# Performance work log

Hardware: AMD Instinct MI355X
Metric: run time of the kernel (lower is better)

The kernel has to match this reference:

```python
import jax, jax.numpy as jnp
import numpy as np

B, S, SK = 4, 1024, 1024
Q_IN, KV_IN = 1024, 1024
G, DQ, DV = 16, 64, 64
OUT = Q_IN
EPS = 1e-5


def setup_inputs() -> dict:
    key = jax.random.key(0)
    ks = jax.random.split(key, 12)
    s_q = 1.0 / np.sqrt(Q_IN)
    s_kv = 1.0 / np.sqrt(KV_IN)
    s_p = 1.0 / np.sqrt(G * DV)
    return {
        "Q": jax.random.normal(ks[0], (B, S, Q_IN), jnp.float32),
        "KV": jax.random.normal(ks[1], (B, SK, KV_IN), jnp.float32),
        "Wq": jax.random.normal(ks[2], (G * DQ, Q_IN), jnp.float32) * s_q,
        "bq": jax.random.normal(ks[3], (G * DQ,), jnp.float32) * s_q,
        "Wk": jax.random.normal(ks[4], (G * DQ, KV_IN), jnp.float32) * s_kv,
        "bk": jax.random.normal(ks[5], (G * DQ,), jnp.float32) * s_kv,
        "Wv": jax.random.normal(ks[6], (G * DV, KV_IN), jnp.float32) * s_kv,
        "bv": jax.random.normal(ks[7], (G * DV,), jnp.float32) * s_kv,
        "Wp": jax.random.normal(ks[8], (OUT, G * DV), jnp.float32) * s_p,
        "bp": jax.random.normal(ks[9], (OUT,), jnp.float32) * s_p,
        "gamma": jnp.ones((OUT,), jnp.float32),
        "beta": jnp.zeros((OUT,), jnp.float32),
    }


def reference(Q, KV, Wq, bq, Wk, bk, Wv, bv, Wp, bp, gamma, beta):
    b, s, _ = Q.shape
    sk = KV.shape[1]
    inv_sqrt_dim = DQ ** (-0.5)

    # projections
    q = Q @ Wq.T + bq            # [b, s, G*DQ]
    k = KV @ Wk.T + bk           # [b, sk, G*DQ]
    v = KV @ Wv.T + bv           # [b, sk, G*DV]

    # q/k: group is the SLOW axis; v: group is the FAST axis (faithful to source)
    q = q.reshape(b, s, G, DQ)               # [b, s, g, d]
    k = k.reshape(b, sk, G, DQ)              # [b, sk, g, d]
    v = v.reshape(b, sk, DV, G)              # [b, sk, d, g]

    logits = jnp.einsum('bsgd,btgd->bgst', q, k) * inv_sqrt_dim  # [b, g, s, sk]
    scores = jax.nn.softmax(logits, axis=-1)
    attn = jnp.einsum('bgst,btdg->bgsd', scores, v)              # [b, g, s, dv]

    # flatten as (dv, g): feature index = d*G + g  (faithful to source permute)
    attn = attn.transpose(0, 2, 3, 1).reshape(b, s, DV * G)
    out = attn @ Wp.T + bp + Q

    # LayerNorm
    mu = out.mean(axis=-1, keepdims=True)
    var = out.var(axis=-1, keepdims=True)
    out = (out - mu) * jax.lax.rsqrt(var + EPS) * gamma + beta

    return out, scores.reshape(b * G, s, sk)
```

## Files before the change

### kernel.cpp

```cpp
#include <hip/hip_runtime.h>

typedef __attribute__((ext_vector_type(8))) short short8;
typedef __attribute__((ext_vector_type(4))) short s16x4;
typedef __attribute__((ext_vector_type(4))) float f32x4;
typedef __attribute__((ext_vector_type(2))) unsigned u32x2;

static __device__ __forceinline__ short f2bf(float x) {
  union { float f; unsigned u; } v; v.f = x;
  unsigned r = (v.u + 0x7fffu + ((v.u >> 16) & 1u)) >> 16;
  return (short)r;
}
static __device__ __forceinline__ unsigned cvtpk(float lo, float hi) {
  unsigned r;
  asm("v_cvt_pk_bf16_f32 %0, %1, %2" : "=v"(r) : "v"(lo), "v"(hi));
  return r;
}

static __device__ __forceinline__ void gld16(const short* g, short* l) {
  __builtin_amdgcn_global_load_lds(
      (const __attribute__((address_space(1))) unsigned*)g,
      (__attribute__((address_space(3))) unsigned*)l, 16, 0, 0);
}

static __device__ __forceinline__ void conv8(const float* __restrict__ src,
                                             short* __restrict__ dst, int i,
                                             float scale) {
  const f32x4* s = (const f32x4*)(src + (long)i * 8);
  f32x4 a = s[0], b = s[1];
  short8 o;
  o[0] = f2bf(a[0] * scale); o[1] = f2bf(a[1] * scale);
  o[2] = f2bf(a[2] * scale); o[3] = f2bf(a[3] * scale);
  o[4] = f2bf(b[0] * scale); o[5] = f2bf(b[1] * scale);
  o[6] = f2bf(b[2] * scale); o[7] = f2bf(b[3] * scale);
  *(short8*)(dst + (long)i * 8) = o;
}

__global__ __launch_bounds__(256) void prep(
    const float* __restrict__ Q, const float* __restrict__ KV,
    const float* __restrict__ Wq, const float* __restrict__ Wk,
    const float* __restrict__ Wv, const float* __restrict__ Wp,
    const float* __restrict__ bq,
    short* __restrict__ Qb, short* __restrict__ KVb,
    short* __restrict__ Wqb, short* __restrict__ Wkb,
    short* __restrict__ Wvb, short* __restrict__ Wpb,
    float* __restrict__ bqs) {
  const int blk = blockIdx.x, tid = threadIdx.x;
  if (blk < 2048) {
    conv8(Q, Qb, blk * 256 + tid, 1.f);
  } else if (blk < 4096) {
    conv8(KV, KVb, (blk - 2048) * 256 + tid, 1.f);
  } else if (blk < 4608) {
    conv8(Wq, Wqb, (blk - 4096) * 256 + tid, 0.125f);
  } else if (blk < 5120) {
    conv8(Wk, Wkb, (blk - 4608) * 256 + tid, 1.f);
  } else if (blk < 5632) {
    conv8(Wv, Wvb, (blk - 5120) * 256 + tid, 1.f);
  } else if (blk < 6656) {
    __shared__ float row[1024];
    const long o = blk - 5632;
    *(f32x4*)&row[tid * 4] = *(const f32x4*)(Wp + o * 1024 + tid * 4);
    __syncthreads();
    const int f0 = tid * 4;
    s16x4 t;
#pragma unroll
    for (int j = 0; j < 4; ++j) {
      int f = f0 + j;
      t[j] = f2bf(row[((f & 63) << 4) + (f >> 6)]);
    }
    *(s16x4*)(Wpb + o * 1024 + f0) = t;
  } else {
    int i = (blk - 6656) * 256 + tid;
    bqs[i] = bq[i] * 0.125f;
  }
}

template <typename OutT>
static __device__ __forceinline__ void gemm_core(
    const short* __restrict__ A, const short* __restrict__ B,
    OutT* __restrict__ C, const float* __restrict__ bias,
    const float* __restrict__ resid, int bm, int bn, int omode,
    short* Sm) {
  const int tid = threadIdx.x, lane = tid & 63, wave = tid >> 6;
  const int fr = lane & 15, khi = lane >> 4;
  const int wr = wave >> 1, wc = wave & 1;

  f32x4 acc[4][4];
#pragma unroll
  for (int m = 0; m < 4; ++m)
#pragma unroll
    for (int n = 0; n < 4; ++n) acc[m][n] = (f32x4){0.f, 0.f, 0.f, 0.f};

  auto stage = [&](int buf, int k0) {
    short* Asb = Sm + buf * 16384;
    short* Bsb = Asb + 8192;
#pragma unroll
    for (int it = 0; it < 4; ++it) {
      int l = it * 256 + tid;
      int r = l >> 3, c = (l & 7) ^ (r & 7);
      gld16(A + (long)(bm + r) * 1024 + k0 + c * 8, &Asb[l * 8]);
      gld16(B + (long)(bn + r) * 1024 + k0 + c * 8, &Bsb[l * 8]);
    }
  };

  stage(0, 0);
  __syncthreads();
  int cur = 0;
  for (int k0 = 0; k0 < 1024; k0 += 64) {
    if (k0 < 960) stage(cur ^ 1, k0 + 64);
    const short* Asb = Sm + cur * 16384;
    const short* Bsb = Asb + 8192;
#pragma unroll
    for (int ks = 0; ks < 64; ks += 32) {
      const int cc = (ks >> 3) + khi;
      short8 af[4], bf[4];
#pragma unroll
      for (int m = 0; m < 4; ++m) {
        const int ar = wr * 64 + m * 16 + fr;
        af[m] = *(const short8*)&Asb[ar * 64 + ((cc ^ (ar & 7)) * 8)];
      }
#pragma unroll
      for (int n = 0; n < 4; ++n) {
        const int br = wc * 64 + n * 16 + fr;
        bf[n] = *(const short8*)&Bsb[br * 64 + ((cc ^ (br & 7)) * 8)];
      }
#pragma unroll
      for (int m = 0; m < 4; ++m)
#pragma unroll
        for (int n = 0; n < 4; ++n)
          acc[m][n] = __builtin_amdgcn_mfma_f32_16x16x32_bf16(af[m], bf[n],
                                                              acc[m][n], 0, 0, 0);
    }
    __syncthreads();
    cur ^= 1;
  }

  const int col0 = fr, row0 = khi * 4;
  if constexpr (sizeof(OutT) == 2) {
#pragma unroll
    for (int m = 0; m < 4; ++m) {
#pragma unroll
      for (int n = 0; n < 4; ++n) {
        const int dgl = wc * 64 + n * 16 + col0;
        const float bi = bias[bn + dgl];
#pragma unroll
        for (int i = 0; i < 4; ++i) {
          const int tl = wr * 64 + m * 16 + row0 + i;
          const int a = (omode == 1) ? (dgl * 136 + tl) : (tl * 136 + dgl);
          Sm[a] = f2bf(acc[m][n][i] + bi);
        }
      }
    }
    __syncthreads();
    short* Cs = (short*)C;
#pragma unroll
    for (int it = 0; it < 8; ++it) {
      const int ch = it * 256 + tid;
      const int r = ch >> 4, cchunk = ch & 15;
      short8 v8 = *(const short8*)&Sm[r * 136 + cchunk * 8];
      long addr;
      if (omode == 0)
        addr = (long)(bm + r) * 1024 + bn + cchunk * 8;
      else
        addr = ((long)(bm >> 10) << 20) + ((long)(bn + r) << 10) + (bm & 1023) +
               cchunk * 8;
      *(short8*)(Cs + addr) = v8;
    }
  } else {
#pragma unroll
    for (int m = 0; m < 4; ++m) {
#pragma unroll
      for (int n = 0; n < 4; ++n) {
        const int gcol = bn + wc * 64 + n * 16 + col0;
        const float bi = bias[gcol];
#pragma unroll
        for (int i = 0; i < 4; ++i) {
          const int grow = bm + wr * 64 + m * 16 + row0 + i;
          float v = acc[m][n][i] + bi;
          if (resid) v += resid[(long)grow * 1024 + gcol];
          C[(long)grow * 1024 + gcol] = v;
        }
      }
    }
  }
}

__global__ __launch_bounds__(256, 2) void proj_all(
    const short* __restrict__ Qb, const short* __restrict__ KVb,
    const short* __restrict__ Wqb, const short* __restrict__ Wkb,
    const short* __restrict__ Wvb,
    const float* __restrict__ bqs, const float* __restrict__ bk,
    const float* __restrict__ bv,
    short* __restrict__ qb, short* __restrict__ kb, short* __restrict__ vt) {
  __shared__ short Sm[32768];
  int bid = blockIdx.x;
  int swz = (bid & 7) * 96 + (bid >> 3);
  const int seg = swz >> 8, local = swz & 255;
  const int bm = (local >> 3) * 128, bn = (local & 7) * 128;
  if (seg == 0)
    gemm_core<short>(Qb, Wqb, qb, bqs, nullptr, bm, bn, 0, Sm);
  else if (seg == 1)
    gemm_core<short>(KVb, Wkb, kb, bk, nullptr, bm, bn, 0, Sm);
  else
    gemm_core<short>(KVb, Wvb, vt, bv, nullptr, bm, bn, 1, Sm);
}

__global__ __launch_bounds__(256, 2) void out_gemm(
    const short* __restrict__ at, const short* __restrict__ Wpb,
    const float* __restrict__ bp, const float* __restrict__ Q,
    float* __restrict__ pre) {
  __shared__ short Sm[32768];
  int bid = blockIdx.x;
  int swz = (bid & 7) * 32 + (bid >> 3);
  const int bm = (swz >> 3) * 128, bn = (swz & 7) * 128;
  gemm_core<float>(at, Wpb, pre, bp, Q, bm, bn, 0, Sm);
}

__global__ __launch_bounds__(512, 4) void fused_attn(
    const short* __restrict__ qb,
    const short* __restrict__ kb,
    const short* __restrict__ vt,
    float* __restrict__ scores,
    short* __restrict__ at) {
  constexpr int LP = 72;
  __shared__ short Ks[2][64 * 64];
  __shared__ short Vs[2][64 * 64];
  __shared__ short Ps[128 * LP];

  int bid = blockIdx.x;
  bid = (bid & 7) * 64 + (bid >> 3);
  const int z = bid >> 3, b = z >> 4, g = z & 15;
  const int q0 = (bid & 7) * 128;

  const int tid = threadIdx.x, lane = tid & 63, w = tid >> 6;
  const int fr = lane & 15, khi = lane >> 4;
  const long bqk = (long)b << 20;
  const int qr = q0 + w * 16;

  const short* qrow = qb + bqk + (long)(qr + fr) * 1024 + g * 64 + khi * 8;
  const short8 aq0 = *(const short8*)qrow;
  const short8 aq1 = *(const short8*)(qrow + 32);
  const short* kgp = kb + bqk + g * 64;
  const short* vgp = vt + bqk;

  auto stageK = [&](int buf, int t0) {
    int r = tid >> 3, c = (tid & 7) ^ ((tid >> 5) & 7);
    gld16(kgp + (long)(t0 + r) * 1024 + c * 8, &Ks[buf][tid * 8]);
  };
  auto stageV = [&](int buf, int t0) {
    int r = tid >> 3, c = (tid & 7) ^ (r & 7);
    gld16(vgp + ((long)(r * 16 + g) << 10) + t0 + c * 8, &Vs[buf][tid * 8]);
  };

  const int xk = fr & 7;

  float s4[4] = {0.f, 0.f, 0.f, 0.f};
  stageK(0, 0);
  __syncthreads();
  int cur = 0;
  for (int t0 = 0; t0 < 1024; t0 += 64) {
    if (t0 < 960) stageK(cur ^ 1, t0 + 64);
    f32x4 sacc[4];
#pragma unroll
    for (int nf = 0; nf < 4; ++nf) sacc[nf] = (f32x4){0.f, 0.f, 0.f, 0.f};
#pragma unroll
    for (int nf = 0; nf < 4; ++nf) {
      const int r2 = fr * 4 + nf;
      short8 b0 = *(const short8*)&Ks[cur][r2 * 64 + ((khi ^ xk) * 8)];
      short8 b1 = *(const short8*)&Ks[cur][r2 * 64 + (((khi + 4) ^ xk) * 8)];
      sacc[nf] = __builtin_amdgcn_mfma_f32_16x16x32_bf16(aq0, b0, sacc[nf], 0, 0, 0);
      sacc[nf] = __builtin_amdgcn_mfma_f32_16x16x32_bf16(aq1, b1, sacc[nf], 0, 0, 0);
    }
#pragma unroll
    for (int nf = 0; nf < 4; ++nf)
#pragma unroll
      for (int i = 0; i < 4; ++i) s4[i] += __expf(sacc[nf][i]);
    __syncthreads();
    cur ^= 1;
  }
  float inv4[4];
#pragma unroll
  for (int i = 0; i < 4; ++i) {
    float s = s4[i];
    s += __shfl_xor(s, 1);
    s += __shfl_xor(s, 2);
    s += __shfl_xor(s, 4);
    s += __shfl_xor(s, 8);
    inv4[i] = 1.f / s;
  }

  f32x4 pacc[4];
#pragma unroll
  for (int nv = 0; nv < 4; ++nv) pacc[nv] = (f32x4){0.f, 0.f, 0.f, 0.f};

  stageK(0, 0);
  stageV(0, 0);
  __syncthreads();
  cur = 0;
  for (int t0 = 0; t0 < 1024; t0 += 64) {
    if (t0 < 960) {
      stageK(cur ^ 1, t0 + 64);
      stageV(cur ^ 1, t0 + 64);
    }
    f32x4 sacc[4];
#pragma unroll
    for (int nf = 0; nf < 4; ++nf) sacc[nf] = (f32x4){0.f, 0.f, 0.f, 0.f};
#pragma unroll
    for (int nf = 0; nf < 4; ++nf) {
      const int r2 = fr * 4 + nf;
      short8 b0 = *(const short8*)&Ks[cur][r2 * 64 + ((khi ^ xk) * 8)];
      short8 b1 = *(const short8*)&Ks[cur][r2 * 64 + (((khi + 4) ^ xk) * 8)];
      sacc[nf] = __builtin_amdgcn_mfma_f32_16x16x32_bf16(aq0, b0, sacc[nf], 0, 0, 0);
      sacc[nf] = __builtin_amdgcn_mfma_f32_16x16x32_bf16(aq1, b1, sacc[nf], 0, 0, 0);
    }
#pragma unroll
    for (int i = 0; i < 4; ++i) {
      f32x4 o;
#pragma unroll
      for (int nf = 0; nf < 4; ++nf)
        o[nf] = __expf(sacc[nf][i]) * inv4[i];
      const int row = khi * 4 + i;
      __builtin_nontemporal_store(
          o, (f32x4*)&scores[((long)z << 20) + ((long)(qr + row) << 10) + t0 + fr * 4]);
      u32x2 pp;
      pp[0] = cvtpk(o[0], o[1]);
      pp[1] = cvtpk(o[2], o[3]);
      *(u32x2*)&Ps[(w * 16 + row) * LP + fr * 4] = pp;
    }

#pragma unroll
    for (int ks = 0; ks < 64; ks += 32) {
      const int cc = (ks >> 3) + khi;
      short8 ap = *(const short8*)&Ps[(w * 16 + fr) * LP + ks + khi * 8];
#pragma unroll
      for (int nv = 0; nv < 4; ++nv) {
        const int dr = nv * 16 + fr;
        short8 bvv = *(const short8*)&Vs[cur][dr * 64 + ((cc ^ (dr & 7)) * 8)];
        pacc[nv] = __builtin_amdgcn_mfma_f32_16x16x32_bf16(ap, bvv, pacc[nv], 0, 0, 0);
      }
    }
    __syncthreads();
    cur ^= 1;
  }

#pragma unroll
  for (int nv = 0; nv < 4; ++nv)
#pragma unroll
    for (int i = 0; i < 4; ++i)
      Ps[(w * 16 + khi * 4 + i) * LP + nv * 16 + fr] = f2bf(pacc[nv][i]);
  const long atbase = bqk + ((long)qr << 10) + g * 64;
#pragma unroll
  for (int it = 0; it < 2; ++it) {
    const int ch = it * 64 + lane;
    const int row = ch >> 3, fc = ch & 7;
    s16x4 lo = *(const s16x4*)&Ps[(w * 16 + row) * LP + fc * 8];
    s16x4 hi = *(const s16x4*)&Ps[(w * 16 + row) * LP + fc * 8 + 4];
    short8 v8;
    v8[0] = lo[0]; v8[1] = lo[1]; v8[2] = lo[2]; v8[3] = lo[3];
    v8[4] = hi[0]; v8[5] = hi[1]; v8[6] = hi[2]; v8[7] = hi[3];
    *(short8*)(at + atbase + ((long)row << 10) + fc * 8) = v8;
  }
}

__global__ __launch_bounds__(256) void layernorm_rows(const float* __restrict__ X,
                                                      const float* __restrict__ gamma,
                                                      const float* __restrict__ beta,
                                                      float* __restrict__ O) {
  const int row = blockIdx.x * 4 + (threadIdx.x >> 6);
  const int lane = threadIdx.x & 63;
  const float* x = X + (long)row * 1024 + lane * 4;
  f32x4 v[4];
  float s = 0.f, sq = 0.f;
#pragma unroll
  for (int j = 0; j < 4; ++j) {
    v[j] = *(const f32x4*)(x + j * 256);
#pragma unroll
    for (int e = 0; e < 4; ++e) {
      s += v[j][e];
      sq += v[j][e] * v[j][e];
    }
  }
#pragma unroll
  for (int off = 32; off; off >>= 1) {
    s += __shfl_xor(s, off);
    sq += __shfl_xor(sq, off);
  }
  const float mu = s * (1.f / 1024.f);
  const float var = sq * (1.f / 1024.f) - mu * mu;
  const float rstd = rsqrtf(var + 1e-5f);
  float* o = O + (long)row * 1024 + lane * 4;
#pragma unroll
  for (int j = 0; j < 4; ++j) {
    f32x4 g = *(const f32x4*)(gamma + lane * 4 + j * 256);
    f32x4 be = *(const f32x4*)(beta + lane * 4 + j * 256);
    f32x4 r;
#pragma unroll
    for (int e = 0; e < 4; ++e) r[e] = (v[j][e] - mu) * rstd * g[e] + be[e];
    *(f32x4*)(o + j * 256) = r;
  }
}

extern "C" void kernel_launch(void* const* d_in, const int* in_sizes, int n_in,
                              void* d_out, int out_size, void* d_ws, size_t ws_size,
                              hipStream_t stream) {
  const float* Q = (const float*)d_in[0];
  const float* KV = (const float*)d_in[1];
  const float* Wq = (const float*)d_in[2];
  const float* bq = (const float*)d_in[3];
  const float* Wk = (const float*)d_in[4];
  const float* bk = (const float*)d_in[5];
  const float* Wv = (const float*)d_in[6];
  const float* bv = (const float*)d_in[7];
  const float* Wp = (const float*)d_in[8];
  const float* bp = (const float*)d_in[9];
  const float* gamma = (const float*)d_in[10];
  const float* beta = (const float*)d_in[11];

  float* out = (float*)d_out;
  float* scores = out + (long)4 * 1024 * 1024;

  char* ws = (char*)d_ws;
  short* Wqb = (short*)(ws);
  short* Wkb = (short*)(ws + (2L << 20));
  short* Wvb = (short*)(ws + (4L << 20));
  short* Wpb = (short*)(ws + (6L << 20));
  short* qb  = (short*)(ws + (8L << 20));
  short* kb  = (short*)(ws + (16L << 20));
  short* vt  = (short*)(ws + (24L << 20));
  short* at  = (short*)(ws + (32L << 20));
  float* pre = (float*)(ws + (40L << 20));
  short* Qb  = (short*)(ws + (40L << 20));
  short* KVb = (short*)(ws + (48L << 20));
  float* bqs = (float*)(ws + (56L << 20));
  (void)ws_size; (void)in_sizes; (void)n_in; (void)out_size;

  prep<<<6660, 256, 0, stream>>>(Q, KV, Wq, Wk, Wv, Wp, bq,
                                 Qb, KVb, Wqb, Wkb, Wvb, Wpb, bqs);

  proj_all<<<768, 256, 0, stream>>>(Qb, KVb, Wqb, Wkb, Wvb, bqs, bk, bv,
                                    qb, kb, vt);

  fused_attn<<<512, 512, 0, stream>>>(qb, kb, vt, scores, at);

  out_gemm<<<256, 256, 0, stream>>>(at, Wpb, bp, Q, pre);

  layernorm_rows<<<1024, 256, 0, stream>>>(pre, gamma, beta, out);
}
```

Baseline: 162.2 us.

## Cache unnormalized fp16 probabilities in LDS to avoid recomputing QK^T

The attention kernel no longer runs a second QK^T pass. The first pass stores exp(logits) as fp16 into a full 64x1024 LDS row buffer and accumulates row sums from the rounded values. The second pass streams only V, runs fp16 MFMA on P·V, and writes normalized scores from the cached values. V projection output is switched to fp16 to match, blocks now cover 64 query rows with each pair of waves splitting the key/dv columns, and occupancy drops to one block per CU because of the large LDS footprint. The risks are fp16 precision of the stored scores and fewer resident waves to hide latency.

```diff
diff --git a/kernel.cpp b/kernel.cpp
--- a/kernel.cpp
+++ b/kernel.cpp
@@ -4,11 +4,18 @@
 typedef __attribute__((ext_vector_type(4))) short s16x4;
 typedef __attribute__((ext_vector_type(4))) float f32x4;
 typedef __attribute__((ext_vector_type(2))) unsigned u32x2;
+typedef __attribute__((ext_vector_type(2))) __fp16 h2v;
+typedef __attribute__((ext_vector_type(8))) _Float16 half8;
 
 static __device__ __forceinline__ short f2bf(float x) {
   union { float f; unsigned u; } v; v.f = x;
   unsigned r = (v.u + 0x7fffu + ((v.u >> 16) & 1u)) >> 16;
   return (short)r;
+}
+static __device__ __forceinline__ short f2h(float x) {
+  h2v p = __builtin_amdgcn_cvt_pkrtz(x, 0.f);
+  union { h2v v; unsigned u; } c; c.v = p;
+  return (short)(c.u & 0xffffu);
 }
 static __device__ __forceinline__ unsigned cvtpk(float lo, float hi) {
   unsigned r;
@@ -146,7 +153,8 @@
         for (int i = 0; i < 4; ++i) {
           const int tl = wr * 64 + m * 16 + row0 + i;
           const int a = (omode == 1) ? (dgl * 136 + tl) : (tl * 136 + dgl);
-          Sm[a] = f2bf(acc[m][n][i] + bi);
+          const float vv = acc[m][n][i] + bi;
+          Sm[a] = (omode == 1) ? f2h(vv) : f2bf(vv);
         }
       }
     }
@@ -215,28 +223,29 @@
   gemm_core<float>(at, Wpb, pre, bp, Q, bm, bn, 0, Sm);
 }
 
-__global__ __launch_bounds__(512, 4) void fused_attn(
+__global__ __launch_bounds__(512, 1) void fused_attn(
     const short* __restrict__ qb,
     const short* __restrict__ kb,
     const short* __restrict__ vt,
     float* __restrict__ scores,
     short* __restrict__ at) {
-  constexpr int LP = 72;
+  constexpr int LPF = 1032;
+  __shared__ short Pfull[64 * LPF];
   __shared__ short Ks[2][64 * 64];
-  __shared__ short Vs[2][64 * 64];
-  __shared__ short Ps[128 * LP];
+  __shared__ float SxL[128];
+  __shared__ float invL[64];
 
   int bid = blockIdx.x;
-  bid = (bid & 7) * 64 + (bid >> 3);
-  const int z = bid >> 3, b = z >> 4, g = z & 15;
-  const int q0 = (bid & 7) * 128;
+  bid = (bid & 7) * 128 + (bid >> 3);
+  const int z = bid >> 4, b = z >> 4, g = z & 15;
+  const int q0 = (bid & 15) * 64;
 
   const int tid = threadIdx.x, lane = tid & 63, w = tid >> 6;
   const int fr = lane & 15, khi = lane >> 4;
   const long bqk = (long)b << 20;
-  const int qr = q0 + w * 16;
-
-  const short* qrow = qb + bqk + (long)(qr + fr) * 1024 + g * 64 + khi * 8;
+  const int rg = w >> 1, kh = w & 1;
+
+  const short* qrow = qb + bqk + (long)(q0 + rg * 16 + fr) * 1024 + g * 64 + khi * 8;
   const short8 aq0 = *(const short8*)qrow;
   const short8 aq1 = *(const short8*)(qrow + 32);
   const short* kgp = kb + bqk + g * 64;
@@ -248,10 +257,10 @@
   };
   auto stageV = [&](int buf, int t0) {
     int r = tid >> 3, c = (tid & 7) ^ (r & 7);
-    gld16(vgp + ((long)(r * 16 + g) << 10) + t0 + c * 8, &Vs[buf][tid * 8]);
+    gld16(vgp + ((long)(r * 16 + g) << 10) + t0 + c * 8, &Ks[buf][tid * 8]);
   };
 
-  const int xk = fr & 7;
+  const int xk = fr >> 1;
 
   float s4[4] = {0.f, 0.f, 0.f, 0.f};
   stageK(0, 0);
@@ -259,25 +268,29 @@
   int cur = 0;
   for (int t0 = 0; t0 < 1024; t0 += 64) {
     if (t0 < 960) stageK(cur ^ 1, t0 + 64);
-    f32x4 sacc[4];
-#pragma unroll
-    for (int nf = 0; nf < 4; ++nf) sacc[nf] = (f32x4){0.f, 0.f, 0.f, 0.f};
-#pragma unroll
-    for (int nf = 0; nf < 4; ++nf) {
-      const int r2 = fr * 4 + nf;
+    f32x4 sacc[2];
+    sacc[0] = (f32x4){0.f, 0.f, 0.f, 0.f};
+    sacc[1] = (f32x4){0.f, 0.f, 0.f, 0.f};
+#pragma unroll
+    for (int nf = 0; nf < 2; ++nf) {
+      const int r2 = kh * 32 + fr * 2 + nf;
       short8 b0 = *(const short8*)&Ks[cur][r2 * 64 + ((khi ^ xk) * 8)];
       short8 b1 = *(const short8*)&Ks[cur][r2 * 64 + (((khi + 4) ^ xk) * 8)];
       sacc[nf] = __builtin_amdgcn_mfma_f32_16x16x32_bf16(aq0, b0, sacc[nf], 0, 0, 0);
       sacc[nf] = __builtin_amdgcn_mfma_f32_16x16x32_bf16(aq1, b1, sacc[nf], 0, 0, 0);
     }
 #pragma unroll
-    for (int nf = 0; nf < 4; ++nf)
-#pragma unroll
-      for (int i = 0; i < 4; ++i) s4[i] += __expf(sacc[nf][i]);
+    for (int i = 0; i < 4; ++i) {
+      float o0 = __expf(sacc[0][i]);
+      float o1 = __expf(sacc[1][i]);
+      h2v pk = __builtin_amdgcn_cvt_pkrtz(o0, o1);
+      union { h2v v; unsigned u; } c; c.v = pk;
+      *(unsigned*)&Pfull[(rg * 16 + khi * 4 + i) * LPF + t0 + kh * 32 + fr * 2] = c.u;
+      s4[i] += (float)pk[0] + (float)pk[1];
+    }
     __syncthreads();
     cur ^= 1;
   }
-  float inv4[4];
 #pragma unroll
   for (int i = 0; i < 4; ++i) {
     float s = s4[i];
@@ -285,79 +298,76 @@
     s += __shfl_xor(s, 2);
     s += __shfl_xor(s, 4);
     s += __shfl_xor(s, 8);
-    inv4[i] = 1.f / s;
-  }
-
-  f32x4 pacc[4];
-#pragma unroll
-  for (int nv = 0; nv < 4; ++nv) pacc[nv] = (f32x4){0.f, 0.f, 0.f, 0.f};
-
-  stageK(0, 0);
+    s4[i] = s;
+  }
+  if (fr == 0) {
+#pragma unroll
+    for (int i = 0; i < 4; ++i) SxL[w * 16 + khi * 4 + i] = s4[i];
+  }
+  __syncthreads();
+  if (tid < 64) {
+    const int r16 = tid & 15, rgw = (tid >> 4) * 2;
+    invL[tid] = 1.f / (SxL[rgw * 16 + r16] + SxL[(rgw + 1) * 16 + r16]);
+  }
+  __syncthreads();
+
+  f32x4 pacc[2];
+  pacc[0] = (f32x4){0.f, 0.f, 0.f, 0.f};
+  pacc[1] = (f32x4){0.f, 0.f, 0.f, 0.f};
+  float iv[4];
+#pragma unroll
+  for (int i = 0; i < 4; ++i) iv[i] = invL[rg * 16 + khi * 4 + i];
+  const float ivb = invL[tid >> 3];
+  const int srow = tid >> 3, sc8 = tid & 7;
+
   stageV(0, 0);
   __syncthreads();
   cur = 0;
-  for (int t0 = 0; t0 < 1024; t0 += 64) {
-    if (t0 < 960) {
-      stageK(cur ^ 1, t0 + 64);
-      stageV(cur ^ 1, t0 + 64);
-    }
-    f32x4 sacc[4];
-#pragma unroll
-    for (int nf = 0; nf < 4; ++nf) sacc[nf] = (f32x4){0.f, 0.f, 0.f, 0.f};
-#pragma unroll
-    for (int nf = 0; nf < 4; ++nf) {
-      const int r2 = fr * 4 + nf;
-      short8 b0 = *(const short8*)&Ks[cur][r2 * 64 + ((khi ^ xk) * 8)];
-      short8 b1 = *(const short8*)&Ks[cur][r2 * 64 + (((khi + 4) ^ xk) * 8)];
-      sacc[nf] = __builtin_amdgcn_mfma_f32_16x16x32_bf16(aq0, b0, sacc[nf], 0, 0, 0);
-      sacc[nf] = __builtin_amdgcn_mfma_f32_16x16x32_bf16(aq1, b1, sacc[nf], 0, 0, 0);
-    }
-#pragma unroll
-    for (int i = 0; i < 4; ++i) {
-      f32x4 o;
-#pragma unroll
-      for (int nf = 0; nf < 4; ++nf)
-        o[nf] = __expf(sacc[nf][i]) * inv4[i];
-      const int row = khi * 4 + i;
-      __builtin_nontemporal_store(
-          o, (f32x4*)&scores[((long)z << 20) + ((long)(qr + row) << 10) + t0 + fr * 4]);
-      u32x2 pp;
-      pp[0] = cvtpk(o[0], o[1]);
-      pp[1] = cvtpk(o[2], o[3]);
-      *(u32x2*)&Ps[(w * 16 + row) * LP + fr * 4] = pp;
-    }
-
-#pragma unroll
-    for (int ks = 0; ks < 64; ks += 32) {
-      const int cc = (ks >> 3) + khi;
-      short8 ap = *(const short8*)&Ps[(w * 16 + fr) * LP + ks + khi * 8];
-#pragma unroll
-      for (int nv = 0; nv < 4; ++nv) {
-        const int dr = nv * 16 + fr;
-        short8 bvv = *(const short8*)&Vs[cur][dr * 64 + ((cc ^ (dr & 7)) * 8)];
-        pacc[nv] = __builtin_amdgcn_mfma_f32_16x16x32_bf16(ap, bvv, pacc[nv], 0, 0, 0);
-      }
+  for (int tv = 0; tv < 1024; tv += 64) {
+    if (tv < 960) stageV(cur ^ 1, tv + 64);
+#pragma unroll
+    for (int kk = 0; kk < 2; ++kk) {
+      half8 ap = *(const half8*)&Pfull[(rg * 16 + fr) * LPF + tv + kk * 32 + khi * 8];
+      const int cc = kk * 4 + khi;
+#pragma unroll
+      for (int nv = 0; nv < 2; ++nv) {
+        const int dr = kh * 32 + nv * 16 + fr;
+        half8 bvv = *(const half8*)&Ks[cur][dr * 64 + ((cc ^ (dr & 7)) * 8)];
+        pacc[nv] = __builtin_amdgcn_mfma_f32_16x16x32_f16(ap, bvv, pacc[nv], 0, 0, 0);
+      }
+    }
+    {
+      half8 hv = *(const half8*)&Pfull[srow * LPF + tv + sc8 * 8];
+      f32x4 oa, ob;
+#pragma unroll
+      for (int j = 0; j < 4; ++j) {
+        oa[j] = (float)hv[j] * ivb;
+        ob[j] = (float)hv[j + 4] * ivb;
+      }
+      float* sp = &scores[((long)z << 20) + ((long)(q0 + srow) << 10) + tv + sc8 * 8];
+      __builtin_nontemporal_store(oa, (f32x4*)sp);
+      __builtin_nontemporal_store(ob, (f32x4*)(sp + 4));
     }
     __syncthreads();
     cur ^= 1;
   }
 
-#pragma unroll
-  for (int nv = 0; nv < 4; ++nv)
+  short* bounce = (short*)Ks;
+#pragma unroll
+  for (int nv = 0; nv < 2; ++nv)
 #pragma unroll
     for (int i = 0; i < 4; ++i)
-      Ps[(w * 16 + khi * 4 + i) * LP + nv * 16 + fr] = f2bf(pacc[nv][i]);
-  const long atbase = bqk + ((long)qr << 10) + g * 64;
-#pragma unroll
-  for (int it = 0; it < 2; ++it) {
-    const int ch = it * 64 + lane;
-    const int row = ch >> 3, fc = ch & 7;
-    s16x4 lo = *(const s16x4*)&Ps[(w * 16 + row) * LP + fc * 8];
-    s16x4 hi = *(const s16x4*)&Ps[(w * 16 + row) * LP + fc * 8 + 4];
+      bounce[(rg * 16 + khi * 4 + i) * 72 + kh * 32 + nv * 16 + fr] =
+          f2bf(pacc[nv][i] * iv[i]);
+  __syncthreads();
+  {
+    const int row = tid >> 3, fc = tid & 7;
+    s16x4 lo = *(const s16x4*)&bounce[row * 72 + fc * 8];
+    s16x4 hi = *(const s16x4*)&bounce[row * 72 + fc * 8 + 4];
     short8 v8;
     v8[0] = lo[0]; v8[1] = lo[1]; v8[2] = lo[2]; v8[3] = lo[3];
     v8[4] = hi[0]; v8[5] = hi[1]; v8[6] = hi[2]; v8[7] = hi[3];
-    *(short8*)(at + atbase + ((long)row << 10) + fc * 8) = v8;
+    *(short8*)(at + bqk + ((long)(q0 + row) << 10) + g * 64 + fc * 8) = v8;
   }
 }
 
@@ -439,7 +449,7 @@
   proj_all<<<768, 256, 0, stream>>>(Qb, KVb, Wqb, Wkb, Wvb, bqs, bk, bv,
                                     qb, kb, vt);
 
-  fused_attn<<<512, 512, 0, stream>>>(qb, kb, vt, scores, at);
+  fused_attn<<<1024, 512, 0, stream>>>(qb, kb, vt, scores, at);
 
   out_gemm<<<256, 256, 0, stream>>>(at, Wpb, bp, Q, pre);
 
```

Result: slower. 174.5 us (+7.6%).
